# Kernel optimization log

Hardware: AMD Instinct MI355X
Metric: run time of the kernel (lower is better)

Reference implementation:

```python
import jax, jax.numpy as jnp
import numpy as np
from jax import lax

EPS = 1e-4       # BatchNorm eps from module
THRESHOLD = 0.0  # TernaryActive threshold (default)

B, C_IN, H, W = 16, 32, 256, 256
C_OUT, K, STRIDE, PAD = 32, 3, 1, 1


def setup_inputs() -> dict:
    key = jax.random.key(0)
    ks = jax.random.split(key, 7)
    x = jax.random.normal(ks[0], (B, C_IN, H, W), dtype=jnp.float32)
    bn_gamma = jax.random.normal(ks[1], (C_IN,), dtype=jnp.float32) * 0.1 + 1.0
    bn_beta = jax.random.normal(ks[2], (C_IN,), dtype=jnp.float32) * 0.1
    bn_mean = jax.random.normal(ks[3], (C_IN,), dtype=jnp.float32) * 0.1
    bn_var = jax.random.uniform(ks[4], (C_IN,), dtype=jnp.float32, minval=0.5, maxval=1.5)
    fan_in = C_IN * K * K
    bound = 1.0 / np.sqrt(fan_in)
    conv_w = jax.random.uniform(ks[5], (C_OUT, C_IN, K, K), dtype=jnp.float32, minval=-bound, maxval=bound)
    conv_b = jax.random.uniform(ks[6], (C_OUT,), dtype=jnp.float32, minval=-bound, maxval=bound)
    return {"x": x, "bn_gamma": bn_gamma, "bn_beta": bn_beta,
            "bn_mean": bn_mean, "bn_var": bn_var,
            "conv_w": conv_w, "conv_b": conv_b}


def _ternary(x):
    # torch: output[x >= thr] = 1, then output[x <= -thr] = -1 (le overrides ge)
    return jnp.where(x <= -THRESHOLD, -1.0,
                     jnp.where(x >= THRESHOLD, 1.0, 0.0)).astype(x.dtype)


def reference(x, bn_gamma, bn_beta, bn_mean, bn_var, conv_w, conv_b):
    # BatchNorm2d (inference form with running stats), per-channel over C
    inv = bn_gamma / jnp.sqrt(bn_var + EPS)
    xh = x * inv[None, :, None, None] + (bn_beta - bn_mean * inv)[None, :, None, None]
    # Ternary quantize {-1, 0, 1}
    q = _ternary(xh)
    # Conv2d 3x3, stride 1, pad 1 (NCHW / OIHW)
    y = lax.conv_general_dilated(q, conv_w, window_strides=(STRIDE, STRIDE),
                                 padding=[(PAD, PAD), (PAD, PAD)],
                                 dimension_numbers=("NCHW", "OIHW", "NCHW"))
    y = y + conv_b[None, :, None, None]
    # ReLU
    return jnp.maximum(y, 0.0)
```

## Files before the change

### kernel.cpp

```cpp
#include <hip/hip_runtime.h>


#define B_    16
#define H_    256
#define W_    256
#define SW    32
#define YC    32
#define ROWB  2304
#define NITEM 576

typedef __bf16 bf16x8 __attribute__((ext_vector_type(8)));
typedef float  f32x4  __attribute__((ext_vector_type(4)));
union FragCast { int4 i; bf16x8 b; };

__device__ __forceinline__ unsigned short f2bf(float f) {
    union { float f; unsigned u; } c; c.f = f;
    unsigned u = c.u;
    u += 0x7FFFu + ((u >> 16) & 1u);
    return (unsigned short)(u >> 16);
}

__device__ __forceinline__ unsigned short quant1(float v, float sc, float sh) {
    float xh = __fadd_rn(__fmul_rn(v, sc), sh);
    return (xh <= 0.0f) ? (unsigned short)0xBF80u
         : ((xh >= 0.0f) ? (unsigned short)0x3F80u : (unsigned short)0u);
}

__launch_bounds__(256, 4)
__global__ void tbconv_kernel(const float* __restrict__ x,
                              const float* __restrict__ bn_g,
                              const float* __restrict__ bn_b,
                              const float* __restrict__ bn_m,
                              const float* __restrict__ bn_v,
                              const float* __restrict__ conv_w,
                              const float* __restrict__ conv_b,
                              float* __restrict__ out)
{
    __shared__ __align__(16) unsigned char sQ[4 * ROWB];
    __shared__ __align__(16) unsigned int  sW[4608];
    __shared__ float sScale[32], sShift[32];

    const int tid = threadIdx.x;
    const int bx  = blockIdx.x;
    const int strip = bx & 7;
    const int yc    = (bx >> 3) & 7;
    const int b     = bx >> 6;
    const int x0 = strip * SW;
    const int y0 = yc * YC;

    if (tid < 32) {
        float s = __fdiv_rn(bn_g[tid], __fsqrt_rn(__fadd_rn(bn_v[tid], 1e-4f)));
        sScale[tid] = s;
        sShift[tid] = __fsub_rn(bn_b[tid], __fmul_rn(bn_m[tid], s));
    }
    for (int j = tid; j < 4608; j += 256) {
        int cp = j & 15, co = (j >> 4) & 31, t = j >> 9;
        float w0 = conv_w[(co * 32 + 2 * cp)     * 9 + t];
        float w1 = conv_w[(co * 32 + 2 * cp + 1) * 9 + t];
        sW[j] = (unsigned)f2bf(w0) | ((unsigned)f2bf(w1) << 16);
    }
    __syncthreads();

    const float* lp[3];
    int   lw0[3], lw1[3];
    float lsc[3], lsh[3];
    bool  lxok[3];
    const bool lv2 = (tid < 64);
    #pragma unroll
    for (int j = 0; j < 3; ++j) {
        int i = tid + 256 * j; if (i >= NITEM) i = 0;
        int ci = i / 18, pr = i - 18 * ci;
        int gx = x0 - 2 + 2 * pr;
        bool xok = (gx >= 0) && (gx < W_);
        int gxc = (gx < 0) ? 0 : ((gx > 254) ? 254 : gx);
        lp[j]   = x + (((size_t)(b * 32 + ci)) << 16) + gxc;
        lxok[j] = xok;
        int hx0 = 2 * pr - 1, hx1 = 2 * pr;
        int hc0 = (hx0 < 0)  ? 34 : hx0;
        int hc1 = (hx1 > 33) ? 35 : hx1;
        int q = ci >> 3, cl = ci & 7;
        lw0[j] = ((hc0 * 4 + (q ^ ((hc0 >> 1) & 3))) << 4) + cl * 2;
        lw1[j] = ((hc1 * 4 + (q ^ ((hc1 >> 1) & 3))) << 4) + cl * 2;
        lsc[j] = sScale[ci]; lsh[j] = sShift[ci];
    }

    const int lane = tid & 63, wave = tid >> 6;
    const int quad = lane >> 4, n = lane & 15;
    const int ct = wave >> 1, xh = wave & 1;
    const int xl = xh * 16 + n;

    FragCast fA[9];
    #pragma unroll
    for (int t = 0; t < 9; ++t)
        fA[t].i = *(const int4*)((const char*)sW + ((t * 32 + ct * 16 + n) * 32 + quad * 8) * 2);

    int dsoff[3];
    #pragma unroll
    for (int kw = 0; kw < 3; ++kw) {
        int hx = xl + kw;
        dsoff[kw] = (hx * 4 + (quad ^ ((hx >> 1) & 3))) << 4;
    }

    float  bias[4];
    size_t obase[4];
    #pragma unroll
    for (int r = 0; r < 4; ++r) {
        int co = ct * 16 + quad * 4 + r;
        bias[r]  = conv_b[co];
        obase[r] = (((size_t)(b * 32 + co)) << 16) + ((size_t)y0 << 8) + (x0 + xl);
    }

    float2 v[3];
    auto load_row = [&](int gy) {
        bool yok = ((unsigned)gy < (unsigned)H_);
        #pragma unroll
        for (int j = 0; j < 3; ++j) {
            v[j] = make_float2(0.f, 0.f);
            if (yok && (j < 2 || lv2))
                v[j] = *(const float2*)(lp[j] + (gy << 8));
        }
    };
    auto scatter = [&](int gy, int slot) {
        bool yok = ((unsigned)gy < (unsigned)H_);
        char* rowp = (char*)sQ + slot * ROWB;
        #pragma unroll
        for (int j = 0; j < 3; ++j) {
            if (j < 2 || lv2) {
                unsigned short q0 = 0, q1 = 0;
                if (yok && lxok[j]) {
                    q0 = quant1(v[j].x, lsc[j], lsh[j]);
                    q1 = quant1(v[j].y, lsc[j], lsh[j]);
                }
                *(unsigned short*)(rowp + lw0[j]) = q0;
                *(unsigned short*)(rowp + lw1[j]) = q1;
            }
        }
    };

    load_row(y0 - 1); scatter(y0 - 1, 3);
    load_row(y0);     scatter(y0,     0);
    load_row(y0 + 1); scatter(y0 + 1, 1);
    load_row(y0 + 2);
    __syncthreads();

    for (int t8 = 0; t8 < 8; ++t8) {
        #pragma unroll
        for (int u = 0; u < 4; ++u) {
            const int yy = t8 * 4 + u;
            const int y  = y0 + yy;

            f32x4 acc[3];
            #pragma unroll
            for (int kh = 0; kh < 3; ++kh) {
                const int sb = ((u + 3 + kh) & 3) * ROWB;
                f32x4 a = {0.f, 0.f, 0.f, 0.f};
                #pragma unroll
                for (int kw = 0; kw < 3; ++kw) {
                    FragCast fB;
                    fB.i = *(const int4*)((const char*)sQ + sb + dsoff[kw]);
                    a = __builtin_amdgcn_mfma_f32_16x16x32_bf16(fA[kh * 3 + kw].b, fB.b, a, 0, 0, 0);
                }
                acc[kh] = a;
            }

            if (yy <= 30) scatter(y + 2, (u + 2) & 3);
            __syncthreads();

            #pragma unroll
            for (int r = 0; r < 4; ++r) {
                float s = __fadd_rn(__fadd_rn(acc[0][r], acc[1][r]),
                                    __fadd_rn(acc[2][r], bias[r]));
                out[obase[r] + (yy << 8)] = fmaxf(s, 0.f);
            }
            if (yy <= 29) load_row(y + 3);
        }
    }
}

extern "C" void kernel_launch(void* const* d_in, const int* in_sizes, int n_in,
                              void* d_out, int out_size, void* d_ws, size_t ws_size,
                              hipStream_t stream) {
    const float* x     = (const float*)d_in[0];
    const float* gamma = (const float*)d_in[1];
    const float* beta  = (const float*)d_in[2];
    const float* mean  = (const float*)d_in[3];
    const float* var   = (const float*)d_in[4];
    const float* w     = (const float*)d_in[5];
    const float* bias  = (const float*)d_in[6];
    float* o = (float*)d_out;

    dim3 grid(B_ * 8 * 8);
    dim3 block(256);
    hipLaunchKernelGGL(tbconv_kernel, grid, block, 0, stream,
                       x, gamma, beta, mean, var, w, bias, o);
}
```

Baseline: 272.5 us.

## Halve row chunk, double-buffer row prefetch, load weights directly into registers

Each block now covers 16 rows instead of 32, so the grid doubles, and occupancy hint rises to 6 blocks per CU. The shared-memory weight staging is removed; each lane builds its bf16 MFMA A-fragments straight from global memory. Input loading is reorganised: each thread handles two channels with packed 32-bit LDS writes, separate edge threads fetch the halo columns, and rows are prefetched two ahead with two register buffers. This aims for more latency hiding and less LDS traffic. In exchange, halo rows are reloaded more often and weights are fetched redundantly per block.

```diff
diff --git a/kernel.cpp b/kernel.cpp
--- a/kernel.cpp
+++ b/kernel.cpp
@@ -4,10 +4,7 @@
 #define B_    16
 #define H_    256
 #define W_    256
-#define SW    32
-#define YC    32
-#define ROWB  2304
-#define NITEM 576
+#define ROWB  2176
 
 typedef __bf16 bf16x8 __attribute__((ext_vector_type(8)));
 typedef float  f32x4  __attribute__((ext_vector_type(4)));
@@ -20,13 +17,16 @@
     return (unsigned short)(u >> 16);
 }
 
-__device__ __forceinline__ unsigned short quant1(float v, float sc, float sh) {
+__device__ __forceinline__ unsigned quant1(float v, float sc, float sh) {
     float xh = __fadd_rn(__fmul_rn(v, sc), sh);
-    return (xh <= 0.0f) ? (unsigned short)0xBF80u
-         : ((xh >= 0.0f) ? (unsigned short)0x3F80u : (unsigned short)0u);
+    return (xh <= 0.0f) ? 0xBF80u : ((xh >= 0.0f) ? 0x3F80u : 0u);
 }
 
-__launch_bounds__(256, 4)
+__device__ __forceinline__ int chunkaddr(int hx, int q) {
+    return (hx * 4 + (q ^ ((hx >> 1) & 3))) << 4;
+}
+
+__launch_bounds__(256, 6)
 __global__ void tbconv_kernel(const float* __restrict__ x,
                               const float* __restrict__ bn_g,
                               const float* __restrict__ bn_b,
@@ -37,117 +37,117 @@
                               float* __restrict__ out)
 {
     __shared__ __align__(16) unsigned char sQ[4 * ROWB];
-    __shared__ __align__(16) unsigned int  sW[4608];
     __shared__ float sScale[32], sShift[32];
 
     const int tid = threadIdx.x;
     const int bx  = blockIdx.x;
     const int strip = bx & 7;
-    const int yc    = (bx >> 3) & 7;
-    const int b     = bx >> 6;
-    const int x0 = strip * SW;
-    const int y0 = yc * YC;
+    const int yc    = (bx >> 3) & 15;
+    const int b     = bx >> 7;
+    const int x0 = strip * 32;
+    const int y0 = yc * 16;
 
     if (tid < 32) {
         float s = __fdiv_rn(bn_g[tid], __fsqrt_rn(__fadd_rn(bn_v[tid], 1e-4f)));
         sScale[tid] = s;
         sShift[tid] = __fsub_rn(bn_b[tid], __fmul_rn(bn_m[tid], s));
     }
-    for (int j = tid; j < 4608; j += 256) {
-        int cp = j & 15, co = (j >> 4) & 31, t = j >> 9;
-        float w0 = conv_w[(co * 32 + 2 * cp)     * 9 + t];
-        float w1 = conv_w[(co * 32 + 2 * cp + 1) * 9 + t];
-        sW[j] = (unsigned)f2bf(w0) | ((unsigned)f2bf(w1) << 16);
-    }
-    __syncthreads();
-
-    const float* lp[3];
-    int   lw0[3], lw1[3];
-    float lsc[3], lsh[3];
-    bool  lxok[3];
-    const bool lv2 = (tid < 64);
-    #pragma unroll
-    for (int j = 0; j < 3; ++j) {
-        int i = tid + 256 * j; if (i >= NITEM) i = 0;
-        int ci = i / 18, pr = i - 18 * ci;
-        int gx = x0 - 2 + 2 * pr;
-        bool xok = (gx >= 0) && (gx < W_);
-        int gxc = (gx < 0) ? 0 : ((gx > 254) ? 254 : gx);
-        lp[j]   = x + (((size_t)(b * 32 + ci)) << 16) + gxc;
-        lxok[j] = xok;
-        int hx0 = 2 * pr - 1, hx1 = 2 * pr;
-        int hc0 = (hx0 < 0)  ? 34 : hx0;
-        int hc1 = (hx1 > 33) ? 35 : hx1;
-        int q = ci >> 3, cl = ci & 7;
-        lw0[j] = ((hc0 * 4 + (q ^ ((hc0 >> 1) & 3))) << 4) + cl * 2;
-        lw1[j] = ((hc1 * 4 + (q ^ ((hc1 >> 1) & 3))) << 4) + cl * 2;
-        lsc[j] = sScale[ci]; lsh[j] = sShift[ci];
-    }
 
     const int lane = tid & 63, wave = tid >> 6;
     const int quad = lane >> 4, n = lane & 15;
     const int ct = wave >> 1, xh = wave & 1;
     const int xl = xh * 16 + n;
+    const int co_a = ct * 16 + n;
 
     FragCast fA[9];
     #pragma unroll
-    for (int t = 0; t < 9; ++t)
-        fA[t].i = *(const int4*)((const char*)sW + ((t * 32 + ct * 16 + n) * 32 + quad * 8) * 2);
+    for (int t = 0; t < 9; ++t) fA[t].i = make_int4(0, 0, 0, 0);
+    {
+        const float* wb = conv_w + (co_a * 32 + quad * 8) * 9;
+        #pragma unroll
+        for (int j = 0; j < 8; ++j) {
+            #pragma unroll
+            for (int t = 0; t < 9; ++t) {
+                unsigned v = (unsigned)f2bf(wb[j * 9 + t]) << ((j & 1) * 16);
+                int* pi = (int*)&fA[t];
+                pi[j >> 1] |= (int)v;
+            }
+        }
+    }
+    __syncthreads();
+
+    const int ci2 = tid >> 4, pr0 = tid & 15;
+    const float* lpI = x + (((size_t)(b * 32 + 2 * ci2)) << 16) + (x0 + 2 * pr0);
+    const float scA = sScale[2 * ci2],     shA = sShift[2 * ci2];
+    const float scB = sScale[2 * ci2 + 1], shB = sShift[2 * ci2 + 1];
+    const int lwA = chunkaddr(2 * pr0 + 1, ci2 >> 2) + (ci2 & 3) * 4;
+    const int lwB = chunkaddr(2 * pr0 + 2, ci2 >> 2) + (ci2 & 3) * 4;
+
+    const bool isEdge = (tid < 32);
+    const int  side   = (tid >> 4) & 1;
+    const int  ci2e   = tid & 15;
+    const int  gxe    = side ? (x0 + 32) : (x0 - 1);
+    const bool exok   = (gxe >= 0) && (gxe < W_);
+    const int  gxec   = (gxe < 0) ? 0 : ((gxe > 255) ? 255 : gxe);
+    const float* lpE  = x + (((size_t)(b * 32 + 2 * ci2e)) << 16) + gxec;
+    const float sceA = sScale[2 * ci2e],     sheA = sShift[2 * ci2e];
+    const float sceB = sScale[2 * ci2e + 1], sheB = sShift[2 * ci2e + 1];
+    const int  lwE   = chunkaddr(side ? 33 : 0, ci2e >> 2) + (ci2e & 3) * 4;
 
     int dsoff[3];
     #pragma unroll
-    for (int kw = 0; kw < 3; ++kw) {
-        int hx = xl + kw;
-        dsoff[kw] = (hx * 4 + (quad ^ ((hx >> 1) & 3))) << 4;
-    }
+    for (int kw = 0; kw < 3; ++kw)
+        dsoff[kw] = chunkaddr(xl + kw, quad);
 
-    float  bias[4];
-    size_t obase[4];
+    float bias[4];
     #pragma unroll
-    for (int r = 0; r < 4; ++r) {
-        int co = ct * 16 + quad * 4 + r;
-        bias[r]  = conv_b[co];
-        obase[r] = (((size_t)(b * 32 + co)) << 16) + ((size_t)y0 << 8) + (x0 + xl);
-    }
+    for (int r = 0; r < 4; ++r) bias[r] = conv_b[ct * 16 + quad * 4 + r];
+    float* outp = out + (((size_t)(b * 32 + ct * 16 + quad * 4)) << 16)
+                      + ((size_t)y0 << 8) + (x0 + xl);
 
-    float2 v[3];
-    auto load_row = [&](int gy) {
-        bool yok = ((unsigned)gy < (unsigned)H_);
-        #pragma unroll
-        for (int j = 0; j < 3; ++j) {
-            v[j] = make_float2(0.f, 0.f);
-            if (yok && (j < 2 || lv2))
-                v[j] = *(const float2*)(lp[j] + (gy << 8));
-        }
-    };
-    auto scatter = [&](int gy, int slot) {
-        bool yok = ((unsigned)gy < (unsigned)H_);
-        char* rowp = (char*)sQ + slot * ROWB;
-        #pragma unroll
-        for (int j = 0; j < 3; ++j) {
-            if (j < 2 || lv2) {
-                unsigned short q0 = 0, q1 = 0;
-                if (yok && lxok[j]) {
-                    q0 = quant1(v[j].x, lsc[j], lsh[j]);
-                    q1 = quant1(v[j].y, lsc[j], lsh[j]);
-                }
-                *(unsigned short*)(rowp + lw0[j]) = q0;
-                *(unsigned short*)(rowp + lw1[j]) = q1;
+    struct Buf { float2 a, b; float ea, eb; };
+    Buf buf0, buf1;
+
+    auto load_row = [&](int gy, Buf& v) {
+        v.a = make_float2(0.f, 0.f); v.b = make_float2(0.f, 0.f);
+        v.ea = 0.f; v.eb = 0.f;
+        if ((unsigned)gy < (unsigned)H_) {
+            v.a = *(const float2*)(lpI + (gy << 8));
+            v.b = *(const float2*)(lpI + 65536 + (gy << 8));
+            if (isEdge) {
+                v.ea = lpE[gy << 8];
+                v.eb = lpE[65536 + (gy << 8)];
             }
         }
     };
+    auto scatter = [&](int gy, int slot, const Buf& v) {
+        const bool yok = (unsigned)gy < (unsigned)H_;
+        char* rp = (char*)sQ + slot * ROWB;
+        unsigned d0 = 0, d1 = 0, de = 0;
+        if (yok) {
+            d0 = quant1(v.a.x, scA, shA) | (quant1(v.b.x, scB, shB) << 16);
+            d1 = quant1(v.a.y, scA, shA) | (quant1(v.b.y, scB, shB) << 16);
+        }
+        *(unsigned*)(rp + lwA) = d0;
+        *(unsigned*)(rp + lwB) = d1;
+        if (isEdge) {
+            if (yok && exok)
+                de = quant1(v.ea, sceA, sheA) | (quant1(v.eb, sceB, sheB) << 16);
+            *(unsigned*)(rp + lwE) = de;
+        }
+    };
 
-    load_row(y0 - 1); scatter(y0 - 1, 3);
-    load_row(y0);     scatter(y0,     0);
-    load_row(y0 + 1); scatter(y0 + 1, 1);
-    load_row(y0 + 2);
+    load_row(y0 - 1, buf0); scatter(y0 - 1, 3, buf0);
+    load_row(y0,     buf0); scatter(y0,     0, buf0);
+    load_row(y0 + 1, buf0); scatter(y0 + 1, 1, buf0);
+    load_row(y0 + 2, buf0);
+    load_row(y0 + 3, buf1);
     __syncthreads();
 
-    for (int t8 = 0; t8 < 8; ++t8) {
+    for (int t4 = 0; t4 < 4; ++t4) {
         #pragma unroll
         for (int u = 0; u < 4; ++u) {
-            const int yy = t8 * 4 + u;
-            const int y  = y0 + yy;
+            const int yy = t4 * 4 + u;
 
             f32x4 acc[3];
             #pragma unroll
@@ -163,16 +163,17 @@
                 acc[kh] = a;
             }
 
-            if (yy <= 30) scatter(y + 2, (u + 2) & 3);
+            Buf& vb = (u & 1) ? buf1 : buf0;
+            if (yy <= 14) scatter(y0 + yy + 2, (u + 2) & 3, vb);
+            if (yy <= 12) load_row(y0 + yy + 4, vb);
             __syncthreads();
 
             #pragma unroll
             for (int r = 0; r < 4; ++r) {
                 float s = __fadd_rn(__fadd_rn(acc[0][r], acc[1][r]),
                                     __fadd_rn(acc[2][r], bias[r]));
-                out[obase[r] + (yy << 8)] = fmaxf(s, 0.f);
+                outp[(size_t)r * 65536 + (yy << 8)] = fmaxf(s, 0.f);
             }
-            if (yy <= 29) load_row(y + 3);
         }
     }
 }
@@ -189,7 +190,7 @@
     const float* bias  = (const float*)d_in[6];
     float* o = (float*)d_out;
 
-    dim3 grid(B_ * 8 * 8);
+    dim3 grid(B_ * 8 * 16);
     dim3 block(256);
     hipLaunchKernelGGL(tbconv_kernel, grid, block, 0, stream,
                        x, gamma, beta, mean, var, w, bias, o);
```

Measured after the change: 388.6 us. 1.43x slower.
